# Kernel optimization log

Hardware: AMD Instinct MI355X
Metric: run time of the kernel (lower is better)

The kernel has to match this reference:

```python
import jax, jax.numpy as jnp
import numpy as np
from jax import lax

GROUPS = 32


def setup_inputs() -> dict:
    key = jax.random.key(0)
    ks = jax.random.split(key, 5)
    b, c, l = 16, 512, 8192
    cg = c // GROUPS
    x = jax.random.normal(ks[0], (b, c, l), dtype=jnp.float32)
    w1 = jax.random.normal(ks[1], (cg, cg, 1), dtype=jnp.float32) * (1.0 / np.sqrt(cg))
    b1 = jax.random.normal(ks[2], (cg,), dtype=jnp.float32) * 0.01
    w3 = jax.random.normal(ks[3], (cg, cg, 3), dtype=jnp.float32) * (1.0 / np.sqrt(3 * cg))
    b3 = jax.random.normal(ks[4], (cg,), dtype=jnp.float32) * 0.01
    return {"x": x, "w1": w1, "b1": b1, "w3": w3, "b3": b3}


def _conv1d(x, w, b, pad):
    # x: (N, C, L), w: (O, I, K) -> (N, O, L)
    y = lax.conv_general_dilated(x, w, window_strides=(1,), padding=pad,
                                 dimension_numbers=("NCH", "OIH", "NCH"))
    return y + b[None, :, None]


def reference(x, w1, b1, w3, b3):
    b, c, l = x.shape
    cg = c // GROUPS
    gx = x.reshape(b * GROUPS, cg, l)                      # (bg, cg, l)
    x1 = _conv1d(gx, w1, b1, "VALID")                       # 1x1 conv
    x2 = _conv1d(gx, w3, b3, "SAME")                        # 1x3 conv, pad=1
    # adaptive avg pool to length 1 == mean over l; softmax over channel axis
    a1 = jax.nn.softmax(x1.mean(axis=-1), axis=-1)          # (bg, cg)
    a2 = jax.nn.softmax(x2.mean(axis=-1), axis=-1)          # (bg, cg)
    weights = jnp.einsum("gc,gcl->gl", a1, x2) + jnp.einsum("gc,gcl->gl", a2, x1)
    out = gx * jax.nn.sigmoid(weights)[:, None, :]
    return out.reshape(b, c, l)
```

## Files before the change

### kernel.cpp

```cpp
#include <hip/hip_runtime.h>

#define LLEN 8192
#define CG 16
#define NG 512

typedef float f32x4 __attribute__((ext_vector_type(4)));

__global__ __launch_bounds__(1024) void sumprep_kernel(const float* __restrict__ x,
                                                       const float* __restrict__ w1,
                                                       const float* __restrict__ b1,
                                                       const float* __restrict__ w3,
                                                       const float* __restrict__ b3,
                                                       float* __restrict__ vw) {
    int g    = blockIdx.x;
    int wave = threadIdx.x >> 6;
    int lane = threadIdx.x & 63;
    __shared__ float S_lds[CG], F_lds[CG], L_lds[CG];

    const float4* xr = reinterpret_cast<const float4*>(x + (size_t)(g * CG + wave) * LLEN);
    float s = 0.f;
    #pragma unroll
    for (int k = 0; k < 32; ++k) {
        float4 v = xr[k * 64 + lane];
        s += (v.x + v.y) + (v.z + v.w);
    }
    #pragma unroll
    for (int off = 32; off; off >>= 1)
        s += __shfl_down(s, off, 64);
    if (lane == 0) S_lds[wave] = s;
    if (threadIdx.x < CG) {
        size_t rb = (size_t)(g * CG + threadIdx.x) * LLEN;
        F_lds[threadIdx.x] = x[rb];
        L_lds[threadIdx.x] = x[rb + (LLEN - 1)];
    }
    __syncthreads();

    if (wave == 0) {
        int i = lane & 15;
        const float invL = 1.0f / (float)LLEN;
        float s1 = 0.f, s2 = 0.f;
        #pragma unroll
        for (int k = 0; k < CG; ++k) {
            float Sk = S_lds[k], Fk = F_lds[k], Lk = L_lds[k];
            s1 += w1[i * CG + k] * Sk;
            const float* w = &w3[(i * CG + k) * 3];
            s2 += w[0] * (Sk - Lk) + w[1] * Sk + w[2] * (Sk - Fk);
        }
        float m1 = s1 * invL + b1[i];
        float m2 = s2 * invL + b3[i];

        float mx1 = m1, mx2 = m2;
        #pragma unroll
        for (int off = 8; off; off >>= 1) {
            mx1 = fmaxf(mx1, __shfl_xor(mx1, off, 16));
            mx2 = fmaxf(mx2, __shfl_xor(mx2, off, 16));
        }
        float e1 = __expf(m1 - mx1), e2 = __expf(m2 - mx2);
        float d1 = e1, d2 = e2;
        #pragma unroll
        for (int off = 8; off; off >>= 1) {
            d1 += __shfl_xor(d1, off, 16);
            d2 += __shfl_xor(d2, off, 16);
        }
        float a1 = e1 / d1, a2 = e2 / d2;

        float cb = a1 * b3[i] + a2 * b1[i];
        #pragma unroll
        for (int off = 8; off; off >>= 1) cb += __shfl_xor(cb, off, 16);

        float v0 = 0.f, v1v = 0.f, v2 = 0.f;
        #pragma unroll
        for (int k = 0; k < CG; ++k) {
            float a1k = __shfl(a1, k, 16);
            float a2k = __shfl(a2, k, 16);
            const float* w = &w3[(k * CG + i) * 3];
            v0  += a1k * w[0];
            v1v += a1k * w[1] + a2k * w1[k * CG + i];
            v2  += a1k * w[2];
        }
        if (lane < 16) {
            float* outv = &vw[g * 64];
            outv[i]      = v0;
            outv[16 + i] = v1v;
            outv[32 + i] = v2;
            if (lane == 0) outv[48] = cb;
        }
    }
}

__global__ __launch_bounds__(256) void apply_kernel(const float* __restrict__ x,
                                                    const float* __restrict__ vw,
                                                    float* __restrict__ out) {
    int wave = (blockIdx.x * 256 + threadIdx.x) >> 6;
    int lane = threadIdx.x & 63;
    int g  = wave >> 5;
    int c0 = (wave & 31) * 256;
    const float* vp = &vw[g * 64];

    const float cb = vp[48];
    float w0 = cb, w1a = cb, w2a = cb, w3a = cb;
    float4 xv[CG];
    #pragma unroll
    for (int i = 0; i < CG; ++i) {
        size_t rb = ((size_t)(g * CG + i)) * LLEN + c0;
        float4 v = *reinterpret_cast<const float4*>(x + rb + 4 * lane);
        xv[i] = v;
        float le = 0.f, re = 0.f;
        if (c0 > 0)            le = x[rb - 1];
        if (c0 + 256 < LLEN)   re = x[rb + 256];
        float fl = __shfl_up(v.w, 1, 64);
        if (lane == 0)  fl = le;
        float fr = __shfl_down(v.x, 1, 64);
        if (lane == 63) fr = re;
        const float a0 = vp[i], a1 = vp[16 + i], a2 = vp[32 + i];
        w0  += a0 * fl  + a1 * v.x + a2 * v.y;
        w1a += a0 * v.x + a1 * v.y + a2 * v.z;
        w2a += a0 * v.y + a1 * v.z + a2 * v.w;
        w3a += a0 * v.z + a1 * v.w + a2 * fr;
    }
    const float s0 = 1.f / (1.f + __expf(-w0));
    const float s1 = 1.f / (1.f + __expf(-w1a));
    const float s2 = 1.f / (1.f + __expf(-w2a));
    const float s3 = 1.f / (1.f + __expf(-w3a));
    #pragma unroll
    for (int i = 0; i < CG; ++i) {
        size_t rb = ((size_t)(g * CG + i)) * LLEN + c0 + 4 * lane;
        float4 v = xv[i];
        f32x4 o4 = { v.x * s0, v.y * s1, v.z * s2, v.w * s3 };
        __builtin_nontemporal_store(o4, reinterpret_cast<f32x4*>(out + rb));
    }
}

extern "C" void kernel_launch(void* const* d_in, const int* in_sizes, int n_in,
                              void* d_out, int out_size, void* d_ws, size_t ws_size,
                              hipStream_t stream) {
    const float* x  = (const float*)d_in[0];
    const float* w1 = (const float*)d_in[1];
    const float* b1 = (const float*)d_in[2];
    const float* w3 = (const float*)d_in[3];
    const float* b3 = (const float*)d_in[4];
    float* out = (float*)d_out;
    float* vw  = (float*)d_ws;

    sumprep_kernel<<<NG, 1024, 0, stream>>>(x, w1, b1, w3, b3, vw);
    apply_kernel<<<4096, 256, 0, stream>>>(x, vw, out);
}
```

Measured before the change: 129.0 us.

## Fuse reduction and apply kernels into one per-group block with LDS coefficients

Merges the per-group sum/softmax prep kernel and the apply kernel into a single kernel, where each 1024-thread block first reduces its group's 16 rows, computes the combined conv-weight coefficients into LDS, then applies the sigmoid gating over the same group's data. The second pass walks the rows in reverse order so the most recently read chunks are revisited first and may still be in cache, and it uses nontemporal loads. This removes a kernel launch and the workspace round trip, and the x data may be served from L2/MALL rather than HBM. In exchange each block serialises reduction then apply, and only 512 blocks of 1024 threads are available to hide latency.

New measurement: 232.6 us. 1.8x slower.

```diff
diff --git a/kernel.cpp b/kernel.cpp
--- a/kernel.cpp
+++ b/kernel.cpp
@@ -6,16 +6,17 @@
 
 typedef float f32x4 __attribute__((ext_vector_type(4)));
 
-__global__ __launch_bounds__(1024) void sumprep_kernel(const float* __restrict__ x,
-                                                       const float* __restrict__ w1,
-                                                       const float* __restrict__ b1,
-                                                       const float* __restrict__ w3,
-                                                       const float* __restrict__ b3,
-                                                       float* __restrict__ vw) {
+__global__ __launch_bounds__(1024) void fused_kernel(const float* __restrict__ x,
+                                                     const float* __restrict__ w1,
+                                                     const float* __restrict__ b1,
+                                                     const float* __restrict__ w3,
+                                                     const float* __restrict__ b3,
+                                                     float* __restrict__ out) {
     int g    = blockIdx.x;
     int wave = threadIdx.x >> 6;
     int lane = threadIdx.x & 63;
     __shared__ float S_lds[CG], F_lds[CG], L_lds[CG];
+    __shared__ float V_lds[49];
 
     const float4* xr = reinterpret_cast<const float4*>(x + (size_t)(g * CG + wave) * LLEN);
     float s = 0.f;
@@ -79,55 +80,50 @@
             v2  += a1k * w[2];
         }
         if (lane < 16) {
-            float* outv = &vw[g * 64];
-            outv[i]      = v0;
-            outv[16 + i] = v1v;
-            outv[32 + i] = v2;
-            if (lane == 0) outv[48] = cb;
+            V_lds[i]      = v0;
+            V_lds[16 + i] = v1v;
+            V_lds[32 + i] = v2;
+            if (lane == 0) V_lds[48] = cb;
         }
     }
-}
+    __syncthreads();
 
-__global__ __launch_bounds__(256) void apply_kernel(const float* __restrict__ x,
-                                                    const float* __restrict__ vw,
-                                                    float* __restrict__ out) {
-    int wave = (blockIdx.x * 256 + threadIdx.x) >> 6;
-    int lane = threadIdx.x & 63;
-    int g  = wave >> 5;
-    int c0 = (wave & 31) * 256;
-    const float* vp = &vw[g * 64];
-
-    const float cb = vp[48];
-    float w0 = cb, w1a = cb, w2a = cb, w3a = cb;
-    float4 xv[CG];
-    #pragma unroll
-    for (int i = 0; i < CG; ++i) {
-        size_t rb = ((size_t)(g * CG + i)) * LLEN + c0;
-        float4 v = *reinterpret_cast<const float4*>(x + rb + 4 * lane);
-        xv[i] = v;
-        float le = 0.f, re = 0.f;
-        if (c0 > 0)            le = x[rb - 1];
-        if (c0 + 256 < LLEN)   re = x[rb + 256];
-        float fl = __shfl_up(v.w, 1, 64);
-        if (lane == 0)  fl = le;
-        float fr = __shfl_down(v.x, 1, 64);
-        if (lane == 63) fr = re;
-        const float a0 = vp[i], a1 = vp[16 + i], a2 = vp[32 + i];
-        w0  += a0 * fl  + a1 * v.x + a2 * v.y;
-        w1a += a0 * v.x + a1 * v.y + a2 * v.z;
-        w2a += a0 * v.y + a1 * v.z + a2 * v.w;
-        w3a += a0 * v.z + a1 * v.w + a2 * fr;
-    }
-    const float s0 = 1.f / (1.f + __expf(-w0));
-    const float s1 = 1.f / (1.f + __expf(-w1a));
-    const float s2 = 1.f / (1.f + __expf(-w2a));
-    const float s3 = 1.f / (1.f + __expf(-w3a));
-    #pragma unroll
-    for (int i = 0; i < CG; ++i) {
-        size_t rb = ((size_t)(g * CG + i)) * LLEN + c0 + 4 * lane;
-        float4 v = xv[i];
-        f32x4 o4 = { v.x * s0, v.y * s1, v.z * s2, v.w * s3 };
-        __builtin_nontemporal_store(o4, reinterpret_cast<f32x4*>(out + rb));
+    const float cbv = V_lds[48];
+    #pragma unroll 1
+    for (int rep = 0; rep < 2; ++rep) {
+        int c0 = (31 - wave - 16 * rep) * 256;
+        float w0 = cbv, w1a = cbv, w2a = cbv, w3a = cbv;
+        f32x4 xv[CG];
+        #pragma unroll
+        for (int i = 0; i < CG; ++i) {
+            size_t rb = ((size_t)(g * CG + i)) * LLEN + c0;
+            f32x4 v = __builtin_nontemporal_load(
+                reinterpret_cast<const f32x4*>(x + rb + 4 * lane));
+            xv[i] = v;
+            float le = 0.f, re = 0.f;
+            if (c0 > 0)            le = x[rb - 1];
+            if (c0 + 256 < LLEN)   re = x[rb + 256];
+            float fl = __shfl_up(v.w, 1, 64);
+            if (lane == 0)  fl = le;
+            float fr = __shfl_down(v.x, 1, 64);
+            if (lane == 63) fr = re;
+            const float a0 = V_lds[i], a1 = V_lds[16 + i], a2 = V_lds[32 + i];
+            w0  += a0 * fl  + a1 * v.x + a2 * v.y;
+            w1a += a0 * v.x + a1 * v.y + a2 * v.z;
+            w2a += a0 * v.y + a1 * v.z + a2 * v.w;
+            w3a += a0 * v.z + a1 * v.w + a2 * fr;
+        }
+        const float s0 = 1.f / (1.f + __expf(-w0));
+        const float s1 = 1.f / (1.f + __expf(-w1a));
+        const float s2 = 1.f / (1.f + __expf(-w2a));
+        const float s3 = 1.f / (1.f + __expf(-w3a));
+        #pragma unroll
+        for (int i = 0; i < CG; ++i) {
+            size_t rb = ((size_t)(g * CG + i)) * LLEN + c0 + 4 * lane;
+            f32x4 v = xv[i];
+            f32x4 o4 = { v.x * s0, v.y * s1, v.z * s2, v.w * s3 };
+            __builtin_nontemporal_store(o4, reinterpret_cast<f32x4*>(out + rb));
+        }
     }
 }
 
@@ -140,8 +136,6 @@
     const float* w3 = (const float*)d_in[3];
     const float* b3 = (const float*)d_in[4];
     float* out = (float*)d_out;
-    float* vw  = (float*)d_ws;
 
-    sumprep_kernel<<<NG, 1024, 0, stream>>>(x, w1, b1, w3, b3, vw);
-    apply_kernel<<<4096, 256, 0, stream>>>(x, vw, out);
+    fused_kernel<<<NG, 1024, 0, stream>>>(x, w1, b1, w3, b3, out);
 }
```
